# Performance work log

Hardware: AMD Instinct MI355X
Metric: run time of the kernel (lower is better)

The kernel has to match this reference:

```python
import jax, jax.numpy as jnp
import numpy as np

NN, D, H = 100000, 300, 1024   # nodes, embedding dim, hidden dim
NG, NS = 50000, 25000          # global vocab, sense vocab
B, T = 8, 128                  # batch, sequence length (state carried across all B*T steps)


def setup_inputs() -> dict:
    key = jax.random.key(0)
    ks = jax.random.split(key, 24)
    s = lambda i, shape: (jax.random.normal(ks[i], shape, jnp.float32) * 0.02)
    return {
        "x_idx": jax.random.randint(ks[0], (B, T), 0, NN),
        "X": jax.random.normal(ks[1], (NN, D), jnp.float32) * 0.1,
        "W_z_1": s(2, (D, H)), "U_z_1": s(3, (H, H)),
        "W_r_1": s(4, (D, H)), "U_r_1": s(5, (H, H)),
        "W_1": s(6, (D, H)), "b_W_1": jnp.zeros((H,), jnp.float32),
        "U_1": s(7, (H, H)), "b_U_1": jnp.zeros((H,), jnp.float32),
        "W_z_2": s(8, (H, H)), "U_z_2": s(9, (H, H)),
        "W_r_2": s(10, (H, H)), "U_r_2": s(11, (H, H)),
        "W_2": s(12, (H, H)), "b_W_2": jnp.zeros((H,), jnp.float32),
        "U_2": s(13, (H, H)), "b_U_2": jnp.zeros((H,), jnp.float32),
        "W_g": s(14, (H, NG)), "b_g": jnp.zeros((NG,), jnp.float32),
        "W_s": s(15, (H, NS)), "b_s": jnp.zeros((NS,), jnp.float32),
    }


def reference(x_idx, X, W_z_1, U_z_1, W_r_1, U_r_1, W_1, b_W_1, U_1, b_U_1,
              W_z_2, U_z_2, W_r_2, U_r_2, W_2, b_W_2, U_2, b_U_2,
              W_g, b_g, W_s, b_s):
    # The original loops over every sample of every sequence, carrying memory_h1/h2
    # across the whole batch; only X[x_indices[0]] feeds the GRU (the GAT-projected
    # neighbours are computed but never used). Dropout in eval mode = identity.
    idx = x_idx.reshape(-1)          # [S] flattened step order (seq-major per sample)
    emb = X[idx]                     # [S, D] currentword embeddings

    def step(carry, e):
        h1, h2 = carry
        z1 = jax.nn.sigmoid(e @ W_z_1 + h1 @ U_z_1)
        r1 = jax.nn.sigmoid(e @ W_r_1 + h1 @ U_r_1)
        ht1 = jnp.tanh((e @ W_1 + b_W_1) + ((r1 * h1) @ U_1 + b_U_1))
        h1n = z1 * ht1 + (1.0 - z1) * h1
        z2 = jax.nn.sigmoid(h1n @ W_z_2 + h2 @ U_z_2)
        r2 = jax.nn.sigmoid(h1n @ W_r_2 + h2 @ U_r_2)
        ht2 = jnp.tanh((h1n @ W_2 + b_W_2) + ((r2 * h2) @ U_2 + b_U_2))
        h2n = z2 * ht2 + (1.0 - z2) * h2
        return (h1n, h2n), h2n

    h0 = jnp.zeros((H,), emb.dtype)
    _, hs = jax.lax.scan(step, (h0, h0), emb)        # hs: [S, H]
    logp_g = jax.nn.log_softmax(hs @ W_g + b_g, axis=-1)   # [S, NG]
    logp_s = jax.nn.log_softmax(hs @ W_s + b_s, axis=-1)   # [S, NS]
    return logp_g, logp_s
```

## Files before the change

kernel.cpp:

```cpp
#include <hip/hip_runtime.h>

typedef __attribute__((ext_vector_type(4))) float f32x4;
typedef __attribute__((ext_vector_type(8))) __bf16 bf16x8;
typedef __attribute__((ext_vector_type(4))) unsigned short u16x4;

#define GPAD 40
#define KEEPF(x) asm volatile("" : "+v"(x))
#define PHYS(i) ((i) + (((i) >> 6) << 2))

__device__ unsigned long long g_h1s[1025 * 1024];
__device__ unsigned long long g_rh1[1024];
__device__ unsigned long long g_h2cur[1024];
__device__ unsigned long long g_rh2[1024];
__device__ float g_ExW[1024 * 3072];
__device__ float g_hs2[1024 * 1024];

__device__ __forceinline__ unsigned short f2bf(float x) {
  unsigned u = __builtin_bit_cast(unsigned, x);
  u += 0x7FFFu + ((u >> 16) & 1u);
  return (unsigned short)(u >> 16);
}
__device__ __forceinline__ unsigned long long packtv(unsigned tag, float v) {
  return ((unsigned long long)tag << 32) | (unsigned long long)__builtin_bit_cast(unsigned, v);
}
__device__ __forceinline__ unsigned long long aload(const unsigned long long* p) {
  return __hip_atomic_load(p, __ATOMIC_RELAXED, __HIP_MEMORY_SCOPE_AGENT);
}
__device__ __forceinline__ void astore(unsigned long long* p, unsigned long long v) {
  __hip_atomic_store(p, v, __ATOMIC_RELAXED, __HIP_MEMORY_SCOPE_AGENT);
}
__device__ __forceinline__ float lo32(unsigned long long v) {
  return __builtin_bit_cast(float, (unsigned)v);
}

__global__ void init_kernel() {
  int t = threadIdx.x;
  astore(&g_rh1[t], 0ull);
  astore(&g_h2cur[t], 0ull);
  astore(&g_rh2[t], 0ull);
}

__global__ __launch_bounds__(256, 1) void fused_scan(
    const float* __restrict__ ExW,
    const float* __restrict__ Uz1, const float* __restrict__ Ur1,
    const float* __restrict__ Uw1, const float* __restrict__ bU1,
    const float* __restrict__ Wz2, const float* __restrict__ Wr2,
    const float* __restrict__ Ww2,
    const float* __restrict__ Uz2, const float* __restrict__ Ur2,
    const float* __restrict__ Uw2,
    const float* __restrict__ bW2, const float* __restrict__ bU2,
    float* __restrict__ hs2)
{
  const int tid = threadIdx.x;
  const int wv = tid >> 6, inw = tid & 63;
  __shared__ __align__(16) float h_s[1088];
  __shared__ __align__(16) float rh_s[1088];
  __shared__ __align__(16) float x_s[1088];

  if (blockIdx.x < 64) {
    const int g = blockIdx.x;
    const int c2 = inw >> 4, q = inw & 15;
    const int j = g * 16 + wv * 4 + c2;
    float uz[64], ur[64], uw[64];
#pragma unroll
    for (int i = 0; i < 64; ++i) uz[i] = Uz1[(size_t)(q * 64 + i) * 1024 + j];
#pragma unroll
    for (int i = 0; i < 64; ++i) ur[i] = Ur1[(size_t)(q * 64 + i) * 1024 + j];
#pragma unroll
    for (int i = 0; i < 64; ++i) uw[i] = Uw1[(size_t)(q * 64 + i) * 1024 + j];
#pragma unroll
    for (int i = 0; i < 64; ++i) { KEEPF(uz[i]); KEEPF(ur[i]); KEEPF(uw[i]); }
    const float bu = bU1[j];

    float xz = 0.f, xr = 0.f, xw = 0.f;
    if (q == 0) { xz = ExW[j]; xr = ExW[1024 + j]; xw = ExW[2048 + j]; }

    float zreg = 0.f, hold = 0.f;
    for (int s = 0; s < 1024; ++s) {
      {
        const unsigned long long* sl = g_h1s + (size_t)s * 1024 + tid * 4;
        unsigned long long a0, a1, a2, a3;
        for (;;) {
          a0 = aload(sl); a1 = aload(sl + 1); a2 = aload(sl + 2); a3 = aload(sl + 3);
          unsigned bad = ((unsigned)(a0 >> 32) ^ (unsigned)s) | ((unsigned)(a1 >> 32) ^ (unsigned)s) |
                         ((unsigned)(a2 >> 32) ^ (unsigned)s) | ((unsigned)(a3 >> 32) ^ (unsigned)s);
          if (bad == 0u) break;
          __builtin_amdgcn_s_sleep(1);
        }
        f32x4 v; v.x = lo32(a0); v.y = lo32(a1); v.z = lo32(a2); v.w = lo32(a3);
        *(f32x4*)&h_s[PHYS(tid * 4)] = v;
      }
      __syncthreads();
      if (q == 0) hold = h_s[PHYS(j)];
      float ar_ = 0.f;
      {
        const float* hp = h_s + q * 68;
#pragma unroll
        for (int i2 = 0; i2 < 16; ++i2) {
          f32x4 hv = *(const f32x4*)(hp + i2 * 4);
          ar_ = fmaf(ur[i2 * 4 + 0], hv.x, ar_); ar_ = fmaf(ur[i2 * 4 + 1], hv.y, ar_);
          ar_ = fmaf(ur[i2 * 4 + 2], hv.z, ar_); ar_ = fmaf(ur[i2 * 4 + 3], hv.w, ar_);
        }
      }
      ar_ += __shfl_xor(ar_, 1, 64); ar_ += __shfl_xor(ar_, 2, 64);
      ar_ += __shfl_xor(ar_, 4, 64); ar_ += __shfl_xor(ar_, 8, 64);
      if (q == 0) {
        float r = 1.f / (1.f + __expf(-(ar_ + xr)));
        astore(&g_rh1[j], packtv((unsigned)(s + 1), r * hold));
      }
      float az_ = 0.f;
      {
        const float* hp = h_s + q * 68;
#pragma unroll
        for (int i2 = 0; i2 < 16; ++i2) {
          f32x4 hv = *(const f32x4*)(hp + i2 * 4);
          az_ = fmaf(uz[i2 * 4 + 0], hv.x, az_); az_ = fmaf(uz[i2 * 4 + 1], hv.y, az_);
          az_ = fmaf(uz[i2 * 4 + 2], hv.z, az_); az_ = fmaf(uz[i2 * 4 + 3], hv.w, az_);
        }
      }
      az_ += __shfl_xor(az_, 1, 64); az_ += __shfl_xor(az_, 2, 64);
      az_ += __shfl_xor(az_, 4, 64); az_ += __shfl_xor(az_, 8, 64);
      if (q == 0) zreg = 1.f / (1.f + __expf(-(az_ + xz)));
      float nxz = 0.f, nxr = 0.f, nxw = 0.f;
      if (q == 0 && s < 1023) {
        nxz = ExW[(s + 1) * 3072 + j];
        nxr = ExW[(s + 1) * 3072 + 1024 + j];
        nxw = ExW[(s + 1) * 3072 + 2048 + j];
      }
      {
        const unsigned long long* sl = g_rh1 + tid * 4;
        unsigned long long a0, a1, a2, a3;
        const unsigned tg = (unsigned)(s + 1);
        for (;;) {
          a0 = aload(sl); a1 = aload(sl + 1); a2 = aload(sl + 2); a3 = aload(sl + 3);
          unsigned bad = ((unsigned)(a0 >> 32) ^ tg) | ((unsigned)(a1 >> 32) ^ tg) |
                         ((unsigned)(a2 >> 32) ^ tg) | ((unsigned)(a3 >> 32) ^ tg);
          if (bad == 0u) break;
          __builtin_amdgcn_s_sleep(1);
        }
        f32x4 v; v.x = lo32(a0); v.y = lo32(a1); v.z = lo32(a2); v.w = lo32(a3);
        *(f32x4*)&rh_s[PHYS(tid * 4)] = v;
      }
      __syncthreads();
      float aw_ = 0.f;
      {
        const float* rp = rh_s + q * 68;
#pragma unroll
        for (int i2 = 0; i2 < 16; ++i2) {
          f32x4 rv = *(const f32x4*)(rp + i2 * 4);
          aw_ = fmaf(uw[i2 * 4 + 0], rv.x, aw_); aw_ = fmaf(uw[i2 * 4 + 1], rv.y, aw_);
          aw_ = fmaf(uw[i2 * 4 + 2], rv.z, aw_); aw_ = fmaf(uw[i2 * 4 + 3], rv.w, aw_);
        }
      }
      aw_ += __shfl_xor(aw_, 1, 64); aw_ += __shfl_xor(aw_, 2, 64);
      aw_ += __shfl_xor(aw_, 4, 64); aw_ += __shfl_xor(aw_, 8, 64);
      if (q == 0) {
        float ht = tanhf(aw_ + xw + bu);
        float hn = zreg * ht + (1.f - zreg) * hold;
        astore(&g_h1s[(size_t)(s + 1) * 1024 + j], packtv((unsigned)(s + 1), hn));
      }
      xz = nxz; xr = nxr; xw = nxw;
    }
  } else {
    const int g = blockIdx.x - 64;
    const int c2 = inw >> 5, q = inw & 31;
    const int j = g * 8 + wv * 2 + c2;
    const int sb = q * 32 + ((q >> 1) << 2);
    float uz[32], ur[32], uw[32], wz[32], wr[32], ww[32];
#pragma unroll
    for (int i = 0; i < 32; ++i) uz[i] = Uz2[(size_t)(q * 32 + i) * 1024 + j];
#pragma unroll
    for (int i = 0; i < 32; ++i) ur[i] = Ur2[(size_t)(q * 32 + i) * 1024 + j];
#pragma unroll
    for (int i = 0; i < 32; ++i) uw[i] = Uw2[(size_t)(q * 32 + i) * 1024 + j];
#pragma unroll
    for (int i = 0; i < 32; ++i) wz[i] = Wz2[(size_t)(q * 32 + i) * 1024 + j];
#pragma unroll
    for (int i = 0; i < 32; ++i) wr[i] = Wr2[(size_t)(q * 32 + i) * 1024 + j];
#pragma unroll
    for (int i = 0; i < 32; ++i) ww[i] = Ww2[(size_t)(q * 32 + i) * 1024 + j];
#pragma unroll
    for (int i = 0; i < 32; ++i) {
      KEEPF(uz[i]); KEEPF(ur[i]); KEEPF(uw[i]);
      KEEPF(wz[i]); KEEPF(wr[i]); KEEPF(ww[i]);
    }
    const float bu = bW2[j] + bU2[j];

    float zreg = 0.f, hold = 0.f;
    for (int s = 0; s < 1024; ++s) {
      {
        const unsigned long long* sh = g_h2cur + tid * 4;
        const unsigned long long* sx = g_h1s + (size_t)(s + 1) * 1024 + tid * 4;
        unsigned long long a0, a1, a2, a3, b0, b1, b2, b3;
        const unsigned tg = (unsigned)(s + 1);
        for (;;) {
          a0 = aload(sh); a1 = aload(sh + 1); a2 = aload(sh + 2); a3 = aload(sh + 3);
          b0 = aload(sx); b1 = aload(sx + 1); b2 = aload(sx + 2); b3 = aload(sx + 3);
          unsigned bad = ((unsigned)(a0 >> 32) ^ (unsigned)s) | ((unsigned)(a1 >> 32) ^ (unsigned)s) |
                         ((unsigned)(a2 >> 32) ^ (unsigned)s) | ((unsigned)(a3 >> 32) ^ (unsigned)s) |
                         ((unsigned)(b0 >> 32) ^ tg) | ((unsigned)(b1 >> 32) ^ tg) |
                         ((unsigned)(b2 >> 32) ^ tg) | ((unsigned)(b3 >> 32) ^ tg);
          if (bad == 0u) break;
          __builtin_amdgcn_s_sleep(1);
        }
        f32x4 v; v.x = lo32(a0); v.y = lo32(a1); v.z = lo32(a2); v.w = lo32(a3);
        *(f32x4*)&h_s[PHYS(tid * 4)] = v;
        f32x4 u4; u4.x = lo32(b0); u4.y = lo32(b1); u4.z = lo32(b2); u4.w = lo32(b3);
        *(f32x4*)&x_s[PHYS(tid * 4)] = u4;
      }
      __syncthreads();
      if (q == 0) hold = h_s[PHYS(j)];
      float ar_ = 0.f;
      {
        const float* hp = h_s + sb;
        const float* xp = x_s + sb;
#pragma unroll
        for (int i2 = 0; i2 < 8; ++i2) {
          f32x4 hv = *(const f32x4*)(hp + i2 * 4);
          f32x4 xv = *(const f32x4*)(xp + i2 * 4);
          ar_ = fmaf(ur[i2 * 4 + 0], hv.x, ar_); ar_ = fmaf(ur[i2 * 4 + 1], hv.y, ar_);
          ar_ = fmaf(ur[i2 * 4 + 2], hv.z, ar_); ar_ = fmaf(ur[i2 * 4 + 3], hv.w, ar_);
          ar_ = fmaf(wr[i2 * 4 + 0], xv.x, ar_); ar_ = fmaf(wr[i2 * 4 + 1], xv.y, ar_);
          ar_ = fmaf(wr[i2 * 4 + 2], xv.z, ar_); ar_ = fmaf(wr[i2 * 4 + 3], xv.w, ar_);
        }
      }
      ar_ += __shfl_xor(ar_, 1, 64); ar_ += __shfl_xor(ar_, 2, 64);
      ar_ += __shfl_xor(ar_, 4, 64); ar_ += __shfl_xor(ar_, 8, 64);
      ar_ += __shfl_xor(ar_, 16, 64);
      if (q == 0) {
        float r = 1.f / (1.f + __expf(-ar_));
        astore(&g_rh2[j], packtv((unsigned)(s + 1), r * hold));
      }
      float az_ = 0.f;
      {
        const float* hp = h_s + sb;
        const float* xp = x_s + sb;
#pragma unroll
        for (int i2 = 0; i2 < 8; ++i2) {
          f32x4 hv = *(const f32x4*)(hp + i2 * 4);
          f32x4 xv = *(const f32x4*)(xp + i2 * 4);
          az_ = fmaf(uz[i2 * 4 + 0], hv.x, az_); az_ = fmaf(uz[i2 * 4 + 1], hv.y, az_);
          az_ = fmaf(uz[i2 * 4 + 2], hv.z, az_); az_ = fmaf(uz[i2 * 4 + 3], hv.w, az_);
          az_ = fmaf(wz[i2 * 4 + 0], xv.x, az_); az_ = fmaf(wz[i2 * 4 + 1], xv.y, az_);
          az_ = fmaf(wz[i2 * 4 + 2], xv.z, az_); az_ = fmaf(wz[i2 * 4 + 3], xv.w, az_);
        }
      }
      az_ += __shfl_xor(az_, 1, 64); az_ += __shfl_xor(az_, 2, 64);
      az_ += __shfl_xor(az_, 4, 64); az_ += __shfl_xor(az_, 8, 64);
      az_ += __shfl_xor(az_, 16, 64);
      if (q == 0) zreg = 1.f / (1.f + __expf(-az_));
      {
        const unsigned long long* sl = g_rh2 + tid * 4;
        unsigned long long a0, a1, a2, a3;
        const unsigned tg = (unsigned)(s + 1);
        for (;;) {
          a0 = aload(sl); a1 = aload(sl + 1); a2 = aload(sl + 2); a3 = aload(sl + 3);
          unsigned bad = ((unsigned)(a0 >> 32) ^ tg) | ((unsigned)(a1 >> 32) ^ tg) |
                         ((unsigned)(a2 >> 32) ^ tg) | ((unsigned)(a3 >> 32) ^ tg);
          if (bad == 0u) break;
          __builtin_amdgcn_s_sleep(1);
        }
        f32x4 v; v.x = lo32(a0); v.y = lo32(a1); v.z = lo32(a2); v.w = lo32(a3);
        *(f32x4*)&rh_s[PHYS(tid * 4)] = v;
      }
      __syncthreads();
      float aw_ = 0.f;
      {
        const float* rp = rh_s + sb;
        const float* xp = x_s + sb;
#pragma unroll
        for (int i2 = 0; i2 < 8; ++i2) {
          f32x4 rv = *(const f32x4*)(rp + i2 * 4);
          f32x4 xv = *(const f32x4*)(xp + i2 * 4);
          aw_ = fmaf(uw[i2 * 4 + 0], rv.x, aw_); aw_ = fmaf(uw[i2 * 4 + 1], rv.y, aw_);
          aw_ = fmaf(uw[i2 * 4 + 2], rv.z, aw_); aw_ = fmaf(uw[i2 * 4 + 3], rv.w, aw_);
          aw_ = fmaf(ww[i2 * 4 + 0], xv.x, aw_); aw_ = fmaf(ww[i2 * 4 + 1], xv.y, aw_);
          aw_ = fmaf(ww[i2 * 4 + 2], xv.z, aw_); aw_ = fmaf(ww[i2 * 4 + 3], xv.w, aw_);
        }
      }
      aw_ += __shfl_xor(aw_, 1, 64); aw_ += __shfl_xor(aw_, 2, 64);
      aw_ += __shfl_xor(aw_, 4, 64); aw_ += __shfl_xor(aw_, 8, 64);
      aw_ += __shfl_xor(aw_, 16, 64);
      if (q == 0) {
        float ht = tanhf(aw_ + bu);
        float hn = zreg * ht + (1.f - zreg) * hold;
        astore(&g_h2cur[j], packtv((unsigned)(s + 1), hn));
        hs2[(size_t)s * 1024 + j] = hn;
      }
    }
  }
}

__global__ __launch_bounds__(256, 1) void gemm_mfma(
    const float* __restrict__ A, const int* __restrict__ gidx, int lda,
    const float* __restrict__ B, int ldb,
    const float* __restrict__ bias,
    float* __restrict__ C, int ldc, int N, int K)
{
  __shared__ unsigned short As[128 * GPAD];
  __shared__ unsigned short Bs[128 * GPAD];
  const int tid = threadIdx.x;
  const int lane = tid & 63;
  const int wv = tid >> 6;
  const int wm = wv >> 1, wn = wv & 1;
  const int mbase = blockIdx.y * 128, nbase = blockIdx.x * 128;

  f32x4 acc[4][4];
#pragma unroll
  for (int i = 0; i < 4; ++i)
#pragma unroll
    for (int qq = 0; qq < 4; ++qq) acc[i][qq] = (f32x4){0.f, 0.f, 0.f, 0.f};

  const int ar = tid >> 1, ak = (tid & 1) * 16;
  const float* Arow;
  {
    int m = mbase + ar;
    long long gr = gidx ? (long long)gidx[m] : (long long)m;
    Arow = A + (size_t)gr * (size_t)lda;
  }
  const int bn = (tid >> 3) * 4;
  const int bk = (tid & 7) * 4;
  const bool nedge = (nbase + 128 > N);

  const int ksteps = (K + 31) >> 5;
  for (int ks = 0; ks < ksteps; ++ks) {
    const int k0 = ks << 5;
    __syncthreads();
    {
      float v[16];
      const int kg = k0 + ak;
      if (kg + 16 <= K) {
#pragma unroll
        for (int qq = 0; qq < 4; ++qq) {
          f32x4 t = *(const f32x4*)(Arow + kg + qq * 4);
          v[qq * 4 + 0] = t.x; v[qq * 4 + 1] = t.y; v[qq * 4 + 2] = t.z; v[qq * 4 + 3] = t.w;
        }
      } else {
#pragma unroll
        for (int i = 0; i < 16; ++i) v[i] = (kg + i < K) ? Arow[kg + i] : 0.f;
      }
#pragma unroll
      for (int qq = 0; qq < 4; ++qq) {
        u16x4 wq;
        wq.x = f2bf(v[qq * 4 + 0]); wq.y = f2bf(v[qq * 4 + 1]);
        wq.z = f2bf(v[qq * 4 + 2]); wq.w = f2bf(v[qq * 4 + 3]);
        *(u16x4*)&As[ar * GPAD + ak + qq * 4] = wq;
      }
    }
    {
      float bv[4][4];
#pragma unroll
      for (int kk = 0; kk < 4; ++kk) {
        int kglob = k0 + bk + kk;
        if (kglob < K) {
          if (!nedge) {
            f32x4 t = *(const f32x4*)(B + (size_t)kglob * (size_t)ldb + nbase + bn);
            bv[kk][0] = t.x; bv[kk][1] = t.y; bv[kk][2] = t.z; bv[kk][3] = t.w;
          } else {
#pragma unroll
            for (int nn = 0; nn < 4; ++nn) {
              int n = nbase + bn + nn;
              bv[kk][nn] = (n < N) ? B[(size_t)kglob * (size_t)ldb + n] : 0.f;
            }
          }
        } else {
          bv[kk][0] = bv[kk][1] = bv[kk][2] = bv[kk][3] = 0.f;
        }
      }
#pragma unroll
      for (int nn = 0; nn < 4; ++nn) {
        u16x4 wq;
        wq.x = f2bf(bv[0][nn]); wq.y = f2bf(bv[1][nn]);
        wq.z = f2bf(bv[2][nn]); wq.w = f2bf(bv[3][nn]);
        *(u16x4*)&Bs[(bn + nn) * GPAD + bk] = wq;
      }
    }
    __syncthreads();
    bf16x8 af[4], bfr[4];
    const int fr = lane & 15, fk = (lane >> 4) * 8;
#pragma unroll
    for (int mf = 0; mf < 4; ++mf)
      af[mf] = *(const bf16x8*)&As[(wm * 64 + mf * 16 + fr) * GPAD + fk];
#pragma unroll
    for (int nf = 0; nf < 4; ++nf)
      bfr[nf] = *(const bf16x8*)&Bs[(wn * 64 + nf * 16 + fr) * GPAD + fk];
#pragma unroll
    for (int mf = 0; mf < 4; ++mf)
#pragma unroll
      for (int nf = 0; nf < 4; ++nf)
        acc[mf][nf] = __builtin_amdgcn_mfma_f32_16x16x32_bf16(af[mf], bfr[nf], acc[mf][nf], 0, 0, 0);
  }
  const int fr = lane & 15, fq = lane >> 4;
#pragma unroll
  for (int nf = 0; nf < 4; ++nf) {
    int col = nbase + wn * 64 + nf * 16 + fr;
    if (col < N) {
      float bb = bias ? bias[col] : 0.f;
#pragma unroll
      for (int mf = 0; mf < 4; ++mf) {
        int row0 = mbase + wm * 64 + mf * 16 + fq * 4;
#pragma unroll
        for (int r = 0; r < 4; ++r)
          C[(size_t)(row0 + r) * (size_t)ldc + col] = acc[mf][nf][r] + bb;
      }
    }
  }
}

__global__ __launch_bounds__(256, 1) void logsoftmax_kernel(float* __restrict__ out) {
  const int row = blockIdx.x;
  float* p; int len;
  if (row < 1024) { p = out + (size_t)row * 50000u; len = 50000; }
  else            { p = out + 51200000ull + (size_t)(row - 1024) * 25000u; len = 25000; }
  const int tid = threadIdx.x;
  __shared__ float mred[4], sred[4];

  float m = -3.4e38f;
  for (int i = tid * 4; i < len; i += 1024) {
    f32x4 v = *(const f32x4*)(p + i);
    m = fmaxf(m, fmaxf(fmaxf(v.x, v.y), fmaxf(v.z, v.w)));
  }
#pragma unroll
  for (int off = 32; off >= 1; off >>= 1) m = fmaxf(m, __shfl_xor(m, off, 64));
  if ((tid & 63) == 0) mred[tid >> 6] = m;
  __syncthreads();
  m = fmaxf(fmaxf(mred[0], mred[1]), fmaxf(mred[2], mred[3]));

  float ssum = 0.f;
  for (int i = tid * 4; i < len; i += 1024) {
    f32x4 v = *(const f32x4*)(p + i);
    ssum += __expf(v.x - m) + __expf(v.y - m) + __expf(v.z - m) + __expf(v.w - m);
  }
#pragma unroll
  for (int off = 32; off >= 1; off >>= 1) ssum += __shfl_xor(ssum, off, 64);
  if ((tid & 63) == 0) sred[tid >> 6] = ssum;
  __syncthreads();
  const float lse = m + logf(sred[0] + sred[1] + sred[2] + sred[3]);

  for (int i = tid * 4; i < len; i += 1024) {
    f32x4 v = *(const f32x4*)(p + i);
    v.x -= lse; v.y -= lse; v.z -= lse; v.w -= lse;
    *(f32x4*)(p + i) = v;
  }
}

extern "C" void kernel_launch(void* const* d_in, const int* in_sizes, int n_in,
                              void* d_out, int out_size, void* d_ws, size_t ws_size,
                              hipStream_t stream) {
  (void)in_sizes; (void)n_in; (void)out_size; (void)d_ws; (void)ws_size;
  const int*   x_idx = (const int*)  d_in[0];
  const float* X     = (const float*)d_in[1];
  const float* W_z_1 = (const float*)d_in[2];
  const float* U_z_1 = (const float*)d_in[3];
  const float* W_r_1 = (const float*)d_in[4];
  const float* U_r_1 = (const float*)d_in[5];
  const float* W_1   = (const float*)d_in[6];
  const float* b_W_1 = (const float*)d_in[7];
  const float* U_1   = (const float*)d_in[8];
  const float* b_U_1 = (const float*)d_in[9];
  const float* W_z_2 = (const float*)d_in[10];
  const float* U_z_2 = (const float*)d_in[11];
  const float* W_r_2 = (const float*)d_in[12];
  const float* U_r_2 = (const float*)d_in[13];
  const float* W_2   = (const float*)d_in[14];
  const float* b_W_2 = (const float*)d_in[15];
  const float* U_2   = (const float*)d_in[16];
  const float* b_U_2 = (const float*)d_in[17];
  const float* W_g   = (const float*)d_in[18];
  const float* b_g   = (const float*)d_in[19];
  const float* W_s   = (const float*)d_in[20];
  const float* b_s   = (const float*)d_in[21];
  float* out = (float*)d_out;

  float *ExW, *hs2;
  unsigned long long* h1s;
  hipGetSymbolAddress((void**)&ExW, HIP_SYMBOL(g_ExW));
  hipGetSymbolAddress((void**)&hs2, HIP_SYMBOL(g_hs2));
  hipGetSymbolAddress((void**)&h1s, HIP_SYMBOL(g_h1s));

  const dim3 blk(256);

  init_kernel<<<dim3(1), dim3(1024), 0, stream>>>();
  hipMemsetAsync(h1s, 0, 1025ull * 1024 * sizeof(unsigned long long), stream);

  gemm_mfma<<<dim3(8, 8), blk, 0, stream>>>(X, x_idx, 300, W_z_1, 1024, nullptr, ExW + 0,    3072, 1024, 300);
  gemm_mfma<<<dim3(8, 8), blk, 0, stream>>>(X, x_idx, 300, W_r_1, 1024, nullptr, ExW + 1024, 3072, 1024, 300);
  gemm_mfma<<<dim3(8, 8), blk, 0, stream>>>(X, x_idx, 300, W_1,   1024, b_W_1,   ExW + 2048, 3072, 1024, 300);

  fused_scan<<<dim3(192), blk, 0, stream>>>(
      ExW, U_z_1, U_r_1, U_1, b_U_1,
      W_z_2, W_r_2, W_2, U_z_2, U_r_2, U_2, b_W_2, b_U_2, hs2);

  gemm_mfma<<<dim3(391, 8), blk, 0, stream>>>(hs2, nullptr, 1024, W_g, 50000, b_g, out,              50000, 50000, 1024);
  gemm_mfma<<<dim3(196, 8), blk, 0, stream>>>(hs2, nullptr, 1024, W_s, 25000, b_s, out + 51200000ll, 25000, 25000, 1024);
  logsoftmax_kernel<<<dim3(2048), blk, 0, stream>>>(out);
}
```

Baseline: 6.803 ms.

## Split layer-2 input projection into its own XCD-pinned role with fast local polling

The persistent scan kernel now launches many blocks and claims roles by XCC id, so layer-1 recurrence, layer-2 recurrence, and the layer-2 input projection (W*h1) each run as 64-block groups, preferably on separate XCDs. The layer-2 input projection becomes a separate pipelined producer that writes tagged results per step, which shortens the layer-2 critical path to only the U matmuls. Polling first reads a fast XCD-local copy with sc0 loads and falls back to the agent-scope copy every few iterations. This adds extra memsets and global buffers, and relies on the hardware placing blocks so that every role fills. If roles land on unexpected XCDs, the fast-copy path and the cross-XCD visibility assumptions could cost extra time.

```diff
diff --git a/kernel.cpp b/kernel.cpp
--- a/kernel.cpp
+++ b/kernel.cpp
@@ -3,15 +3,20 @@
 typedef __attribute__((ext_vector_type(4))) float f32x4;
 typedef __attribute__((ext_vector_type(8))) __bf16 bf16x8;
 typedef __attribute__((ext_vector_type(4))) unsigned short u16x4;
+typedef unsigned long long ull;
 
 #define GPAD 40
 #define KEEPF(x) asm volatile("" : "+v"(x))
 #define PHYS(i) ((i) + (((i) >> 6) << 2))
-
-__device__ unsigned long long g_h1s[1025 * 1024];
-__device__ unsigned long long g_rh1[1024];
-__device__ unsigned long long g_h2cur[1024];
-__device__ unsigned long long g_rh2[1024];
+#define HWREG_XCC_ID ((20) | (0 << 6) | ((4 - 1) << 11))
+
+__device__ ull g_h1f[1024], g_rh1f[1024], g_rh1R[1024];
+__device__ ull g_h2f[1024], g_h2R[1024], g_rh2f[1024], g_rh2R[1024];
+__device__ ull g_h1s[1025 * 1024];
+__device__ ull g_x2z[1025 * 1024];
+__device__ ull g_x2r[1025 * 1024];
+__device__ ull g_x2w[1025 * 1024];
+__device__ int g_claim[4];
 __device__ float g_ExW[1024 * 3072];
 __device__ float g_hs2[1024 * 1024];
 
@@ -20,24 +25,62 @@
   u += 0x7FFFu + ((u >> 16) & 1u);
   return (unsigned short)(u >> 16);
 }
-__device__ __forceinline__ unsigned long long packtv(unsigned tag, float v) {
-  return ((unsigned long long)tag << 32) | (unsigned long long)__builtin_bit_cast(unsigned, v);
-}
-__device__ __forceinline__ unsigned long long aload(const unsigned long long* p) {
+__device__ __forceinline__ ull packtv(unsigned tag, float v) {
+  return ((ull)tag << 32) | (ull)__builtin_bit_cast(unsigned, v);
+}
+__device__ __forceinline__ ull aload(const ull* p) {
   return __hip_atomic_load(p, __ATOMIC_RELAXED, __HIP_MEMORY_SCOPE_AGENT);
 }
-__device__ __forceinline__ void astore(unsigned long long* p, unsigned long long v) {
+__device__ __forceinline__ void astore(ull* p, ull v) {
   __hip_atomic_store(p, v, __ATOMIC_RELAXED, __HIP_MEMORY_SCOPE_AGENT);
 }
-__device__ __forceinline__ float lo32(unsigned long long v) {
+__device__ __forceinline__ void fstore(ull* p, ull v) {
+  __hip_atomic_store(p, v, __ATOMIC_RELAXED, __HIP_MEMORY_SCOPE_WORKGROUP);
+}
+__device__ __forceinline__ float lo32(ull v) {
   return __builtin_bit_cast(float, (unsigned)v);
+}
+__device__ __forceinline__ void fload4(const ull* p, ull& a0, ull& a1, ull& a2, ull& a3) {
+  asm volatile("global_load_dwordx2 %0, %4, off sc0\n\t"
+               "global_load_dwordx2 %1, %4, off offset:8 sc0\n\t"
+               "global_load_dwordx2 %2, %4, off offset:16 sc0\n\t"
+               "global_load_dwordx2 %3, %4, off offset:24 sc0\n\t"
+               "s_waitcnt vmcnt(0)"
+               : "=&v"(a0), "=&v"(a1), "=&v"(a2), "=&v"(a3)
+               : "v"(p) : "memory");
+}
+__device__ __forceinline__ unsigned tagbad4(ull a0, ull a1, ull a2, ull a3, unsigned tg) {
+  return ((unsigned)(a0 >> 32) ^ tg) | ((unsigned)(a1 >> 32) ^ tg) |
+         ((unsigned)(a2 >> 32) ^ tg) | ((unsigned)(a3 >> 32) ^ tg);
+}
+__device__ __forceinline__ f32x4 poll4_fs(const ull* fp, const ull* sp, unsigned tg) {
+  ull a0, a1, a2, a3; int it = 0;
+  for (;;) {
+    fload4(fp, a0, a1, a2, a3);
+    if (!tagbad4(a0, a1, a2, a3, tg)) break;
+    if ((it & 7) == 7) {
+      ull c0 = aload(sp), c1 = aload(sp + 1), c2 = aload(sp + 2), c3 = aload(sp + 3);
+      if (!tagbad4(c0, c1, c2, c3, tg)) { a0 = c0; a1 = c1; a2 = c2; a3 = c3; break; }
+    }
+    ++it; __builtin_amdgcn_s_sleep(1);
+  }
+  f32x4 v; v.x = lo32(a0); v.y = lo32(a1); v.z = lo32(a2); v.w = lo32(a3); return v;
+}
+__device__ __forceinline__ f32x4 poll4_s(const ull* sp, unsigned tg) {
+  ull a0, a1, a2, a3;
+  for (;;) {
+    a0 = aload(sp); a1 = aload(sp + 1); a2 = aload(sp + 2); a3 = aload(sp + 3);
+    if (!tagbad4(a0, a1, a2, a3, tg)) break;
+    __builtin_amdgcn_s_sleep(2);
+  }
+  f32x4 v; v.x = lo32(a0); v.y = lo32(a1); v.z = lo32(a2); v.w = lo32(a3); return v;
 }
 
 __global__ void init_kernel() {
   int t = threadIdx.x;
-  astore(&g_rh1[t], 0ull);
-  astore(&g_h2cur[t], 0ull);
-  astore(&g_rh2[t], 0ull);
+  g_h1f[t] = 0; g_rh1f[t] = 0; g_rh1R[t] = 0;
+  g_h2f[t] = 0; g_h2R[t] = 0; g_rh2f[t] = 0; g_rh2R[t] = 0;
+  if (t < 4) g_claim[t] = 0;
 }
 
 __global__ __launch_bounds__(256, 1) void fused_scan(
@@ -51,16 +94,33 @@
     const float* __restrict__ bW2, const float* __restrict__ bU2,
     float* __restrict__ hs2)
 {
+  __shared__ int sh_role, sh_rank;
   const int tid = threadIdx.x;
+  if (tid == 0) {
+    int xcd = __builtin_amdgcn_s_getreg(HWREG_XCC_ID) & 7;
+    int pref = (xcd == 0) ? 0 : ((xcd == 1) ? 1 : 2);
+    int role = -1, rk = 0;
+    int s0 = atomicAdd(&g_claim[pref], 1);
+    if (s0 < 64) { role = pref; rk = s0; }
+    else if (blockIdx.x >= 768) {
+      for (int r = 0; r < 3 && role < 0; ++r) {
+        int s2 = atomicAdd(&g_claim[r], 1);
+        if (s2 < 64) { role = r; rk = s2; }
+      }
+    }
+    sh_role = role; sh_rank = rk;
+  }
+  __syncthreads();
+  const int role = sh_role, g = sh_rank;
+  if (role < 0) return;
+
   const int wv = tid >> 6, inw = tid & 63;
+  const int c2 = inw >> 4, q = inw & 15;
+  const int j = g * 16 + wv * 4 + c2;
   __shared__ __align__(16) float h_s[1088];
   __shared__ __align__(16) float rh_s[1088];
-  __shared__ __align__(16) float x_s[1088];
-
-  if (blockIdx.x < 64) {
-    const int g = blockIdx.x;
-    const int c2 = inw >> 4, q = inw & 15;
-    const int j = g * 16 + wv * 4 + c2;
+
+  if (role == 0) {
     float uz[64], ur[64], uw[64];
 #pragma unroll
     for (int i = 0; i < 64; ++i) uz[i] = Uz1[(size_t)(q * 64 + i) * 1024 + j];
@@ -77,19 +137,8 @@
 
     float zreg = 0.f, hold = 0.f;
     for (int s = 0; s < 1024; ++s) {
-      {
-        const unsigned long long* sl = g_h1s + (size_t)s * 1024 + tid * 4;
-        unsigned long long a0, a1, a2, a3;
-        for (;;) {
-          a0 = aload(sl); a1 = aload(sl + 1); a2 = aload(sl + 2); a3 = aload(sl + 3);
-          unsigned bad = ((unsigned)(a0 >> 32) ^ (unsigned)s) | ((unsigned)(a1 >> 32) ^ (unsigned)s) |
-                         ((unsigned)(a2 >> 32) ^ (unsigned)s) | ((unsigned)(a3 >> 32) ^ (unsigned)s);
-          if (bad == 0u) break;
-          __builtin_amdgcn_s_sleep(1);
-        }
-        f32x4 v; v.x = lo32(a0); v.y = lo32(a1); v.z = lo32(a2); v.w = lo32(a3);
-        *(f32x4*)&h_s[PHYS(tid * 4)] = v;
-      }
+      f32x4 hv4 = poll4_fs(g_h1f + tid * 4, g_h1s + (size_t)s * 1024 + tid * 4, (unsigned)s);
+      *(f32x4*)&h_s[PHYS(tid * 4)] = hv4;
       __syncthreads();
       if (q == 0) hold = h_s[PHYS(j)];
       float ar_ = 0.f;
@@ -106,7 +155,9 @@
       ar_ += __shfl_xor(ar_, 4, 64); ar_ += __shfl_xor(ar_, 8, 64);
       if (q == 0) {
         float r = 1.f / (1.f + __expf(-(ar_ + xr)));
-        astore(&g_rh1[j], packtv((unsigned)(s + 1), r * hold));
+        ull pk = packtv((unsigned)(s + 1), r * hold);
+        fstore(&g_rh1f[j], pk);
+        astore(&g_rh1R[j], pk);
       }
       float az_ = 0.f;
       {
@@ -127,20 +178,8 @@
         nxr = ExW[(s + 1) * 3072 + 1024 + j];
         nxw = ExW[(s + 1) * 3072 + 2048 + j];
       }
-      {
-        const unsigned long long* sl = g_rh1 + tid * 4;
-        unsigned long long a0, a1, a2, a3;
-        const unsigned tg = (unsigned)(s + 1);
-        for (;;) {
-          a0 = aload(sl); a1 = aload(sl + 1); a2 = aload(sl + 2); a3 = aload(sl + 3);
-          unsigned bad = ((unsigned)(a0 >> 32) ^ tg) | ((unsigned)(a1 >> 32) ^ tg) |
-                         ((unsigned)(a2 >> 32) ^ tg) | ((unsigned)(a3 >> 32) ^ tg);
-          if (bad == 0u) break;
-          __builtin_amdgcn_s_sleep(1);
-        }
-        f32x4 v; v.x = lo32(a0); v.y = lo32(a1); v.z = lo32(a2); v.w = lo32(a3);
-        *(f32x4*)&rh_s[PHYS(tid * 4)] = v;
-      }
+      f32x4 rv4 = poll4_fs(g_rh1f + tid * 4, g_rh1R + tid * 4, (unsigned)(s + 1));
+      *(f32x4*)&rh_s[PHYS(tid * 4)] = rv4;
       __syncthreads();
       float aw_ = 0.f;
       {
@@ -157,136 +196,158 @@
       if (q == 0) {
         float ht = tanhf(aw_ + xw + bu);
         float hn = zreg * ht + (1.f - zreg) * hold;
-        astore(&g_h1s[(size_t)(s + 1) * 1024 + j], packtv((unsigned)(s + 1), hn));
+        ull pk = packtv((unsigned)(s + 1), hn);
+        fstore(&g_h1f[j], pk);
+        astore(&g_h1s[(size_t)(s + 1) * 1024 + j], pk);
       }
       xz = nxz; xr = nxr; xw = nxw;
     }
-  } else {
-    const int g = blockIdx.x - 64;
-    const int c2 = inw >> 5, q = inw & 31;
-    const int j = g * 8 + wv * 2 + c2;
-    const int sb = q * 32 + ((q >> 1) << 2);
-    float uz[32], ur[32], uw[32], wz[32], wr[32], ww[32];
-#pragma unroll
-    for (int i = 0; i < 32; ++i) uz[i] = Uz2[(size_t)(q * 32 + i) * 1024 + j];
-#pragma unroll
-    for (int i = 0; i < 32; ++i) ur[i] = Ur2[(size_t)(q * 32 + i) * 1024 + j];
-#pragma unroll
-    for (int i = 0; i < 32; ++i) uw[i] = Uw2[(size_t)(q * 32 + i) * 1024 + j];
-#pragma unroll
-    for (int i = 0; i < 32; ++i) wz[i] = Wz2[(size_t)(q * 32 + i) * 1024 + j];
-#pragma unroll
-    for (int i = 0; i < 32; ++i) wr[i] = Wr2[(size_t)(q * 32 + i) * 1024 + j];
-#pragma unroll
-    for (int i = 0; i < 32; ++i) ww[i] = Ww2[(size_t)(q * 32 + i) * 1024 + j];
-#pragma unroll
-    for (int i = 0; i < 32; ++i) {
-      KEEPF(uz[i]); KEEPF(ur[i]); KEEPF(uw[i]);
-      KEEPF(wz[i]); KEEPF(wr[i]); KEEPF(ww[i]);
-    }
+  } else if (role == 1) {
+    float uz[64], ur[64], uw[64];
+#pragma unroll
+    for (int i = 0; i < 64; ++i) uz[i] = Uz2[(size_t)(q * 64 + i) * 1024 + j];
+#pragma unroll
+    for (int i = 0; i < 64; ++i) ur[i] = Ur2[(size_t)(q * 64 + i) * 1024 + j];
+#pragma unroll
+    for (int i = 0; i < 64; ++i) uw[i] = Uw2[(size_t)(q * 64 + i) * 1024 + j];
+#pragma unroll
+    for (int i = 0; i < 64; ++i) { KEEPF(uz[i]); KEEPF(ur[i]); KEEPF(uw[i]); }
     const float bu = bW2[j] + bU2[j];
 
     float zreg = 0.f, hold = 0.f;
     for (int s = 0; s < 1024; ++s) {
-      {
-        const unsigned long long* sh = g_h2cur + tid * 4;
-        const unsigned long long* sx = g_h1s + (size_t)(s + 1) * 1024 + tid * 4;
-        unsigned long long a0, a1, a2, a3, b0, b1, b2, b3;
-        const unsigned tg = (unsigned)(s + 1);
+      float xz = 0.f, xr = 0.f, xw = 0.f;
+      {
+        const ull* fp = g_h2f + tid * 4;
+        const ull* sp = g_h2R + tid * 4;
+        const ull* pz = g_x2z + (size_t)(s + 1) * 1024 + j;
+        const ull* pr = g_x2r + (size_t)(s + 1) * 1024 + j;
+        const ull* pw = g_x2w + (size_t)(s + 1) * 1024 + j;
+        const unsigned tgh = (unsigned)s, tgx = (unsigned)(s + 1);
+        ull a0, a1, a2, a3, b0 = 0, b1 = 0, b2 = 0;
+        bool hok = false, xok = (q != 0);
+        int it = 0;
         for (;;) {
-          a0 = aload(sh); a1 = aload(sh + 1); a2 = aload(sh + 2); a3 = aload(sh + 3);
-          b0 = aload(sx); b1 = aload(sx + 1); b2 = aload(sx + 2); b3 = aload(sx + 3);
-          unsigned bad = ((unsigned)(a0 >> 32) ^ (unsigned)s) | ((unsigned)(a1 >> 32) ^ (unsigned)s) |
-                         ((unsigned)(a2 >> 32) ^ (unsigned)s) | ((unsigned)(a3 >> 32) ^ (unsigned)s) |
-                         ((unsigned)(b0 >> 32) ^ tg) | ((unsigned)(b1 >> 32) ^ tg) |
-                         ((unsigned)(b2 >> 32) ^ tg) | ((unsigned)(b3 >> 32) ^ tg);
-          if (bad == 0u) break;
-          __builtin_amdgcn_s_sleep(1);
-        }
+          if (!hok) {
+            fload4(fp, a0, a1, a2, a3);
+            if (!tagbad4(a0, a1, a2, a3, tgh)) hok = true;
+            else if ((it & 7) == 7) {
+              ull c0 = aload(sp), c1 = aload(sp + 1), c2_ = aload(sp + 2), c3 = aload(sp + 3);
+              if (!tagbad4(c0, c1, c2_, c3, tgh)) { a0 = c0; a1 = c1; a2 = c2_; a3 = c3; hok = true; }
+            }
+          }
+          if (!xok) {
+            b0 = aload(pz); b1 = aload(pr); b2 = aload(pw);
+            unsigned xb = ((unsigned)(b0 >> 32) ^ tgx) | ((unsigned)(b1 >> 32) ^ tgx) |
+                          ((unsigned)(b2 >> 32) ^ tgx);
+            if (!xb) xok = true;
+          }
+          if (hok && xok) break;
+          ++it; __builtin_amdgcn_s_sleep(1);
+        }
+        if (q == 0) { xz = lo32(b0); xr = lo32(b1); xw = lo32(b2); }
         f32x4 v; v.x = lo32(a0); v.y = lo32(a1); v.z = lo32(a2); v.w = lo32(a3);
         *(f32x4*)&h_s[PHYS(tid * 4)] = v;
-        f32x4 u4; u4.x = lo32(b0); u4.y = lo32(b1); u4.z = lo32(b2); u4.w = lo32(b3);
-        *(f32x4*)&x_s[PHYS(tid * 4)] = u4;
       }
       __syncthreads();
       if (q == 0) hold = h_s[PHYS(j)];
       float ar_ = 0.f;
       {
-        const float* hp = h_s + sb;
-        const float* xp = x_s + sb;
-#pragma unroll
-        for (int i2 = 0; i2 < 8; ++i2) {
+        const float* hp = h_s + q * 68;
+#pragma unroll
+        for (int i2 = 0; i2 < 16; ++i2) {
           f32x4 hv = *(const f32x4*)(hp + i2 * 4);
-          f32x4 xv = *(const f32x4*)(xp + i2 * 4);
           ar_ = fmaf(ur[i2 * 4 + 0], hv.x, ar_); ar_ = fmaf(ur[i2 * 4 + 1], hv.y, ar_);
           ar_ = fmaf(ur[i2 * 4 + 2], hv.z, ar_); ar_ = fmaf(ur[i2 * 4 + 3], hv.w, ar_);
-          ar_ = fmaf(wr[i2 * 4 + 0], xv.x, ar_); ar_ = fmaf(wr[i2 * 4 + 1], xv.y, ar_);
-          ar_ = fmaf(wr[i2 * 4 + 2], xv.z, ar_); ar_ = fmaf(wr[i2 * 4 + 3], xv.w, ar_);
         }
       }
       ar_ += __shfl_xor(ar_, 1, 64); ar_ += __shfl_xor(ar_, 2, 64);
       ar_ += __shfl_xor(ar_, 4, 64); ar_ += __shfl_xor(ar_, 8, 64);
-      ar_ += __shfl_xor(ar_, 16, 64);
       if (q == 0) {
-        float r = 1.f / (1.f + __expf(-ar_));
-        astore(&g_rh2[j], packtv((unsigned)(s + 1), r * hold));
+        float r = 1.f / (1.f + __expf(-(ar_ + xr)));
+        ull pk = packtv((unsigned)(s + 1), r * hold);
+        fstore(&g_rh2f[j], pk);
+        astore(&g_rh2R[j], pk);
       }
       float az_ = 0.f;
       {
-        const float* hp = h_s + sb;
-        const float* xp = x_s + sb;
-#pragma unroll
-        for (int i2 = 0; i2 < 8; ++i2) {
+        const float* hp = h_s + q * 68;
+#pragma unroll
+        for (int i2 = 0; i2 < 16; ++i2) {
           f32x4 hv = *(const f32x4*)(hp + i2 * 4);
-          f32x4 xv = *(const f32x4*)(xp + i2 * 4);
           az_ = fmaf(uz[i2 * 4 + 0], hv.x, az_); az_ = fmaf(uz[i2 * 4 + 1], hv.y, az_);
           az_ = fmaf(uz[i2 * 4 + 2], hv.z, az_); az_ = fmaf(uz[i2 * 4 + 3], hv.w, az_);
-          az_ = fmaf(wz[i2 * 4 + 0], xv.x, az_); az_ = fmaf(wz[i2 * 4 + 1], xv.y, az_);
-          az_ = fmaf(wz[i2 * 4 + 2], xv.z, az_); az_ = fmaf(wz[i2 * 4 + 3], xv.w, az_);
         }
       }
       az_ += __shfl_xor(az_, 1, 64); az_ += __shfl_xor(az_, 2, 64);
       az_ += __shfl_xor(az_, 4, 64); az_ += __shfl_xor(az_, 8, 64);
-      az_ += __shfl_xor(az_, 16, 64);
-      if (q == 0) zreg = 1.f / (1.f + __expf(-az_));
-      {
-        const unsigned long long* sl = g_rh2 + tid * 4;
-        unsigned long long a0, a1, a2, a3;
-        const unsigned tg = (unsigned)(s + 1);
-        for (;;) {
-          a0 = aload(sl); a1 = aload(sl + 1); a2 = aload(sl + 2); a3 = aload(sl + 3);
-          unsigned bad = ((unsigned)(a0 >> 32) ^ tg) | ((unsigned)(a1 >> 32) ^ tg) |
-                         ((unsigned)(a2 >> 32) ^ tg) | ((unsigned)(a3 >> 32) ^ tg);
-          if (bad == 0u) break;
-          __builtin_amdgcn_s_sleep(1);
-        }
-        f32x4 v; v.x = lo32(a0); v.y = lo32(a1); v.z = lo32(a2); v.w = lo32(a3);
-        *(f32x4*)&rh_s[PHYS(tid * 4)] = v;
-      }
+      if (q == 0) zreg = 1.f / (1.f + __expf(-(az_ + xz)));
+      f32x4 rv4 = poll4_fs(g_rh2f + tid * 4, g_rh2R + tid * 4, (unsigned)(s + 1));
+      *(f32x4*)&rh_s[PHYS(tid * 4)] = rv4;
       __syncthreads();
       float aw_ = 0.f;
       {
-        const float* rp = rh_s + sb;
-        const float* xp = x_s + sb;
-#pragma unroll
-        for (int i2 = 0; i2 < 8; ++i2) {
+        const float* rp = rh_s + q * 68;
+#pragma unroll
+        for (int i2 = 0; i2 < 16; ++i2) {
           f32x4 rv = *(const f32x4*)(rp + i2 * 4);
-          f32x4 xv = *(const f32x4*)(xp + i2 * 4);
           aw_ = fmaf(uw[i2 * 4 + 0], rv.x, aw_); aw_ = fmaf(uw[i2 * 4 + 1], rv.y, aw_);
           aw_ = fmaf(uw[i2 * 4 + 2], rv.z, aw_); aw_ = fmaf(uw[i2 * 4 + 3], rv.w, aw_);
-          aw_ = fmaf(ww[i2 * 4 + 0], xv.x, aw_); aw_ = fmaf(ww[i2 * 4 + 1], xv.y, aw_);
-          aw_ = fmaf(ww[i2 * 4 + 2], xv.z, aw_); aw_ = fmaf(ww[i2 * 4 + 3], xv.w, aw_);
         }
       }
       aw_ += __shfl_xor(aw_, 1, 64); aw_ += __shfl_xor(aw_, 2, 64);
       aw_ += __shfl_xor(aw_, 4, 64); aw_ += __shfl_xor(aw_, 8, 64);
-      aw_ += __shfl_xor(aw_, 16, 64);
       if (q == 0) {
-        float ht = tanhf(aw_ + bu);
+        float ht = tanhf(aw_ + xw + bu);
         float hn = zreg * ht + (1.f - zreg) * hold;
-        astore(&g_h2cur[j], packtv((unsigned)(s + 1), hn));
         hs2[(size_t)s * 1024 + j] = hn;
-      }
+        ull pk = packtv((unsigned)(s + 1), hn);
+        fstore(&g_h2f[j], pk);
+        astore(&g_h2R[j], pk);
+      }
+    }
+  } else {
+    float wz[64], wr[64], ww[64];
+#pragma unroll
+    for (int i = 0; i < 64; ++i) wz[i] = Wz2[(size_t)(q * 64 + i) * 1024 + j];
+#pragma unroll
+    for (int i = 0; i < 64; ++i) wr[i] = Wr2[(size_t)(q * 64 + i) * 1024 + j];
+#pragma unroll
+    for (int i = 0; i < 64; ++i) ww[i] = Ww2[(size_t)(q * 64 + i) * 1024 + j];
+#pragma unroll
+    for (int i = 0; i < 64; ++i) { KEEPF(wz[i]); KEEPF(wr[i]); KEEPF(ww[i]); }
+
+    for (int s = 0; s < 1024; ++s) {
+      f32x4 v = poll4_s(g_h1s + (size_t)(s + 1) * 1024 + tid * 4, (unsigned)(s + 1));
+      *(f32x4*)&h_s[PHYS(tid * 4)] = v;
+      __syncthreads();
+      float az_ = 0.f, ar_ = 0.f, aw_ = 0.f;
+      {
+        const float* hp = h_s + q * 68;
+#pragma unroll
+        for (int i2 = 0; i2 < 16; ++i2) {
+          f32x4 hv = *(const f32x4*)(hp + i2 * 4);
+          az_ = fmaf(wz[i2 * 4 + 0], hv.x, az_); az_ = fmaf(wz[i2 * 4 + 1], hv.y, az_);
+          az_ = fmaf(wz[i2 * 4 + 2], hv.z, az_); az_ = fmaf(wz[i2 * 4 + 3], hv.w, az_);
+          ar_ = fmaf(wr[i2 * 4 + 0], hv.x, ar_); ar_ = fmaf(wr[i2 * 4 + 1], hv.y, ar_);
+          ar_ = fmaf(wr[i2 * 4 + 2], hv.z, ar_); ar_ = fmaf(wr[i2 * 4 + 3], hv.w, ar_);
+          aw_ = fmaf(ww[i2 * 4 + 0], hv.x, aw_); aw_ = fmaf(ww[i2 * 4 + 1], hv.y, aw_);
+          aw_ = fmaf(ww[i2 * 4 + 2], hv.z, aw_); aw_ = fmaf(ww[i2 * 4 + 3], hv.w, aw_);
+        }
+      }
+      az_ += __shfl_xor(az_, 1, 64); az_ += __shfl_xor(az_, 2, 64);
+      az_ += __shfl_xor(az_, 4, 64); az_ += __shfl_xor(az_, 8, 64);
+      ar_ += __shfl_xor(ar_, 1, 64); ar_ += __shfl_xor(ar_, 2, 64);
+      ar_ += __shfl_xor(ar_, 4, 64); ar_ += __shfl_xor(ar_, 8, 64);
+      aw_ += __shfl_xor(aw_, 1, 64); aw_ += __shfl_xor(aw_, 2, 64);
+      aw_ += __shfl_xor(aw_, 4, 64); aw_ += __shfl_xor(aw_, 8, 64);
+      if (q == 0) {
+        const unsigned tg = (unsigned)(s + 1);
+        astore(&g_x2z[(size_t)(s + 1) * 1024 + j], packtv(tg, az_));
+        astore(&g_x2r[(size_t)(s + 1) * 1024 + j], packtv(tg, ar_));
+        astore(&g_x2w[(size_t)(s + 1) * 1024 + j], packtv(tg, aw_));
+      }
+      __syncthreads();
     }
   }
 }
@@ -473,21 +534,27 @@
   float* out = (float*)d_out;
 
   float *ExW, *hs2;
-  unsigned long long* h1s;
+  ull *h1s, *x2z, *x2r, *x2w;
   hipGetSymbolAddress((void**)&ExW, HIP_SYMBOL(g_ExW));
   hipGetSymbolAddress((void**)&hs2, HIP_SYMBOL(g_hs2));
   hipGetSymbolAddress((void**)&h1s, HIP_SYMBOL(g_h1s));
+  hipGetSymbolAddress((void**)&x2z, HIP_SYMBOL(g_x2z));
+  hipGetSymbolAddress((void**)&x2r, HIP_SYMBOL(g_x2r));
+  hipGetSymbolAddress((void**)&x2w, HIP_SYMBOL(g_x2w));
 
   const dim3 blk(256);
 
+  hipMemsetAsync(h1s, 0, 1025ull * 1024 * sizeof(ull), stream);
+  hipMemsetAsync(x2z, 0, 1025ull * 1024 * sizeof(ull), stream);
+  hipMemsetAsync(x2r, 0, 1025ull * 1024 * sizeof(ull), stream);
+  hipMemsetAsync(x2w, 0, 1025ull * 1024 * sizeof(ull), stream);
   init_kernel<<<dim3(1), dim3(1024), 0, stream>>>();
-  hipMemsetAsync(h1s, 0, 1025ull * 1024 * sizeof(unsigned long long), stream);
 
   gemm_mfma<<<dim3(8, 8), blk, 0, stream>>>(X, x_idx, 300, W_z_1, 1024, nullptr, ExW + 0,    3072, 1024, 300);
   gemm_mfma<<<dim3(8, 8), blk, 0, stream>>>(X, x_idx, 300, W_r_1, 1024, nullptr, ExW + 1024, 3072, 1024, 300);
   gemm_mfma<<<dim3(8, 8), blk, 0, stream>>>(X, x_idx, 300, W_1,   1024, b_W_1,   ExW + 2048, 3072, 1024, 300);
 
-  fused_scan<<<dim3(192), blk, 0, stream>>>(
+  fused_scan<<<dim3(1280), blk, 0, stream>>>(
       ExW, U_z_1, U_r_1, U_1, b_U_1,
       W_z_2, W_r_2, W_2, U_z_2, U_r_2, U_2, b_W_2, b_U_2, hs2);
 
```

After: 8.583 ms. 1.26x slower.
